# Kernel optimization log

Measured on AMD Instinct MI355X. Metric: run time of the kernel, lower is better.

Reference implementation:

```python
import jax, jax.numpy as jnp
import numpy as np

# ---- config (mirrors DVE_loss.__init__ defaults used here) ----
POW = 0.5
TEMPERATURE = 1.0
SINK_TAU = 0.3      # sink_tau[1]
SINK_ITERS = 30     # sink_iters[1]
LAMBDA_LC = 1.0
SCALE = 20.0        # F.normalize(...) * 20
EPS = 1e-12


def _l2norm(x, axis):
    n = jnp.sqrt(jnp.sum(x * x, axis=axis, keepdims=True))
    return x / jnp.maximum(n, EPS)


def _sinkhorn(log_alpha, tau, n_iters):
    # log-space Sinkhorn normalization (gumbel_sinkhorn with n_samples=1, no noise)
    la = log_alpha / tau
    def body(i, la):
        la = la - jax.nn.logsumexp(la, axis=1, keepdims=True)  # row normalize
        la = la - jax.nn.logsumexp(la, axis=0, keepdims=True)  # col normalize
        return la
    la = jax.lax.fori_loop(0, n_iters, body, la)
    return jnp.exp(la)


def _per_sample(f1, f2, fa, x1):
    # f1, f2, fa: [N, C] (already normalized * 20); x1: [N, 3]
    N = f1.shape[0]
    dt = f1.dtype

    corr_1a = (f1 @ fa.T) / TEMPERATURE                # [N, N]
    smcorr_1a = jax.nn.softmax(corr_1a, axis=1)
    f1_via_fa_t = smcorr_1a @ fa                        # [N, C] (broadcast-weighted sum)
    corr_1a2 = (f1_via_fa_t @ f2.T) / TEMPERATURE       # [N, N]
    smcorr_1a2 = jax.nn.softmax(corr_1a2, axis=1)

    # no-grad sinkhorn target
    sink = jax.lax.stop_gradient(_sinkhorn(corr_1a2, SINK_TAU, SINK_ITERS))

    # pairwise distance matrix (no-grad): ||xi - xj||^pow
    sq = jnp.sum(x1 * x1, axis=-1)                      # [N]
    d2 = jnp.maximum(sq[:, None] + sq[None, :] - 2.0 * (x1 @ x1.T), 0.0)
    dist = jax.lax.stop_gradient(jnp.sqrt(d2) ** POW)   # [N, N]

    smcorr_12 = jax.nn.softmax((f1 @ f2.T) / TEMPERATURE, axis=1)

    L = dist * smcorr_1a2 + dist * smcorr_12
    loss_b = jnp.sum(L) / N

    perm_to_I_b = 3.0 * jnp.sum(jnp.abs(jnp.eye(N, dtype=dt) - sink)) / N
    Lc_b = 3.0 * jnp.sum(jnp.abs(sink - smcorr_1a2)) / N

    # feature_reconstruction(f1, f1) diagnostic (no-grad)
    g = jax.lax.stop_gradient(f1 @ f1.T)                # [N, N]
    smg = jax.nn.softmax(g / TEMPERATURE, axis=1)
    fv = smg @ jax.lax.stop_gradient(f1)                # [N, C] == (f1 @ smcorr.T).T
    corr2 = fv @ jax.lax.stop_gradient(f1).T            # [N, N] (no temperature div)
    sm2 = jax.nn.softmax(corr2, axis=1)
    d_b = -jnp.sum(jnp.diagonal(sm2)) / N

    match_b = jnp.sum(
        (jnp.argmax(smcorr_1a2, axis=1) == jnp.arange(N)).astype(dt))
    return loss_b, Lc_b, perm_to_I_b, d_b, match_b


def setup_inputs() -> dict:
    key = jax.random.key(0)
    k1, k2 = jax.random.split(key)
    feats = jax.random.normal(k1, (16, 2048, 128), dtype=jnp.float32)
    pc0 = jax.random.normal(k2, (8, 2048, 3), dtype=jnp.float32)
    return {"feats": feats, "pc0": pc0, "epoch": 10}


def reference(feats, pc0, epoch):
    x1 = pc0[..., :3]
    feats1 = feats[0::2]                                # [B, N, C]
    feats2 = feats[1::2]
    B = feats1.shape[0]

    f1 = _l2norm(feats1, axis=-1) * SCALE               # normalize per point
    f2 = _l2norm(feats2, axis=-1) * SCALE
    fa = jnp.roll(f1, -1, axis=0)                       # feats1[(b+1) % B]

    loss_b, Lc_b, perm_b, d_b, match_b = jax.vmap(_per_sample)(f1, f2, fa, x1)

    loss = jnp.sum(loss_b)
    Lc = jnp.sum(Lc_b)
    perm_to_I = jnp.sum(perm_b)
    diff_via_recon = jnp.sum(d_b)
    correct_match = jnp.sum(match_b)

    total_loss = loss + LAMBDA_LC * Lc
    return (total_loss / B, loss / B, Lc / B, perm_to_I / B,
            correct_match / B, diff_via_recon / B)
```

## Files before the change

### kernel.cpp

```cpp
#include <hip/hip_runtime.h>
#include <math.h>

constexpr int B_ = 8;
constexpr int N_ = 2048;
constexpr int D_ = 128;
constexpr long long NDl = (long long)N_ * D_;
constexpr long long NNl = (long long)N_ * N_;
constexpr float INV_TAU = 1.0f / 0.3f;
constexpr float SCALE_ = 20.0f;
constexpr float EPS_ = 1e-12f;

typedef __attribute__((ext_vector_type(8))) short short8;
typedef __attribute__((ext_vector_type(4))) float f32x4;
#define MFMA_BF16 __builtin_amdgcn_mfma_f32_16x16x32_bf16

constexpr size_t FL_F  = (size_t)B_ * NDl;
constexpr size_t FL_NN = (size_t)B_ * NNl;
constexpr size_t FL_V  = (size_t)B_ * N_;

constexpr size_t OFF_SQ   = 0;
constexpr size_t OFF_ROWM = OFF_SQ   + FL_V;
constexpr size_t OFF_ROWZ = OFF_ROWM + FL_V;
constexpr size_t OFF_U0   = OFF_ROWZ + FL_V;
constexpr size_t OFF_V0   = OFF_U0   + FL_V;
constexpr size_t OFF_DIAG = OFF_V0   + FL_V;
constexpr size_t OFF_AV   = OFF_DIAG + FL_V;
constexpr size_t OFF_BV   = OFF_AV   + FL_V;
constexpr size_t OFF_ACC  = OFF_BV   + FL_V;
constexpr size_t OFF_PM   = OFF_ACC  + 16;
constexpr size_t OFF_PS   = OFF_PM   + 32 * FL_V;
constexpr size_t OFF_PT   = OFF_PS   + 32 * FL_V;
constexpr size_t OFF_CP   = OFF_PM;
constexpr size_t OFF_PCM  = OFF_PT;
constexpr size_t OFF_PCS  = OFF_PT + 16 * FL_V;
constexpr size_t OFF_C    = OFF_PM + 128 * FL_V;
constexpr size_t OFF_K    = OFF_C  + FL_NN;
constexpr size_t OFF_BF   = OFF_K  + FL_NN / 2;

__device__ inline float bf2f(unsigned int lo16) {
  return __uint_as_float(lo16 << 16);
}
__device__ inline unsigned int f2bf(float x) {
  unsigned int u = __float_as_uint(x);
  u += 0x7fffu + ((u >> 16) & 1u);
  return (u >> 16) & 0xffffu;
}

__device__ inline void gload16(const unsigned short* g, unsigned short* lbase, int lane) {
#if defined(__has_builtin)
#if __has_builtin(__builtin_amdgcn_global_load_lds)
  __builtin_amdgcn_global_load_lds(
      (const __attribute__((address_space(1))) unsigned int*)g,
      (__attribute__((address_space(3))) unsigned int*)lbase, 16, 0, 0);
  return;
#endif
#endif
  *(uint4*)(lbase + lane * 8) = *(const uint4*)g;
}

__global__ __launch_bounds__(64) void k_norm(const float* __restrict__ feats,
                                             unsigned short* __restrict__ f1hi,
                                             unsigned short* __restrict__ f1lo,
                                             unsigned short* __restrict__ f2hi,
                                             unsigned short* __restrict__ f2lo) {
  int r = blockIdx.x, b = blockIdx.y, which = blockIdx.z;
  const float* src = feats + ((size_t)(2 * b + which)) * NDl + (size_t)r * D_;
  int t = threadIdx.x;
  float2 x = *(const float2*)(src + 2 * t);
  float ss = x.x * x.x + x.y * x.y;
#pragma unroll
  for (int off = 32; off; off >>= 1) ss += __shfl_down(ss, off);
  ss = __shfl(ss, 0);
  float s = SCALE_ / fmaxf(sqrtf(ss), EPS_);
  float y0 = x.x * s, y1 = x.y * s;
  unsigned int h0 = f2bf(y0), h1 = f2bf(y1);
  unsigned int l0 = f2bf(y0 - bf2f(h0)), l1 = f2bf(y1 - bf2f(h1));
  size_t o = (size_t)b * NDl + (size_t)r * D_ + 2 * t;
  unsigned short* hb = (which ? f2hi : f1hi);
  unsigned short* lb = (which ? f2lo : f1lo);
  *(unsigned int*)(hb + o) = h0 | (h1 << 16);
  *(unsigned int*)(lb + o) = l0 | (l1 << 16);
}

__global__ __launch_bounds__(256) void k_transpose(const unsigned short* __restrict__ hi,
                                                   const unsigned short* __restrict__ lo,
                                                   unsigned short* __restrict__ thi,
                                                   unsigned short* __restrict__ tlo) {
  __shared__ unsigned short tile[64][66];
  int rt = blockIdx.x, dt = blockIdx.y, z = blockIdx.z;
  int b = z >> 1;
  const unsigned short* s = ((z & 1) ? lo : hi) + (size_t)b * NDl;
  unsigned short* d = ((z & 1) ? tlo : thi) + (size_t)b * NDl;
  int t = threadIdx.x;
  int r = t >> 2, c0 = (t & 3) * 16;
#pragma unroll
  for (int h = 0; h < 2; ++h) {
    uint4 v = *(const uint4*)(s + (size_t)(rt * 64 + r) * D_ + dt * 64 + c0 + h * 8);
    unsigned short* p = &tile[r][c0 + h * 8];
    p[0] = (unsigned short)v.x; p[1] = (unsigned short)(v.x >> 16);
    p[2] = (unsigned short)v.y; p[3] = (unsigned short)(v.y >> 16);
    p[4] = (unsigned short)v.z; p[5] = (unsigned short)(v.z >> 16);
    p[6] = (unsigned short)v.w; p[7] = (unsigned short)(v.w >> 16);
  }
  __syncthreads();
  int dd = t >> 2, r0 = (t & 3) * 16;
#pragma unroll
  for (int h = 0; h < 2; ++h) {
    unsigned int q[4];
#pragma unroll
    for (int e = 0; e < 4; ++e) {
      unsigned short a0 = tile[r0 + h * 8 + 2 * e][dd];
      unsigned short a1 = tile[r0 + h * 8 + 2 * e + 1][dd];
      q[e] = (unsigned int)a0 | ((unsigned int)a1 << 16);
    }
    uint4 v; v.x = q[0]; v.y = q[1]; v.z = q[2]; v.w = q[3];
    *(uint4*)(d + (size_t)(dt * 64 + dd) * N_ + rt * 64 + r0 + h * 8) = v;
  }
}

__global__ __launch_bounds__(256) void k_sq(const float* __restrict__ pc0,
                                            float* __restrict__ sq) {
  int i = blockIdx.x * 256 + threadIdx.x;
  if (i < B_ * N_) {
    float x = pc0[3 * i], y = pc0[3 * i + 1], z = pc0[3 * i + 2];
    sq[i] = x * x + y * y + z * z;
  }
}

template<bool WRITEC, bool TAU, bool SD, bool DIAG>
__global__ __launch_bounds__(256, 2) void k_mm(
    const unsigned short* __restrict__ Ahi_g, const unsigned short* __restrict__ Alo_g,
    const unsigned short* __restrict__ Bhi_g, const unsigned short* __restrict__ Blo_g,
    float* __restrict__ Cb, int roll,
    float* __restrict__ pms, float* __restrict__ pss, float* __restrict__ pts,
    float* __restrict__ diagb,
    const float* __restrict__ pc0, const float* __restrict__ sqv) {
  int bm = blockIdx.x, bn = blockIdx.y, z = blockIdx.z;
  int zb = (z + roll) & 7;
  const unsigned short* A_hi = Ahi_g + (size_t)z * NDl;
  const unsigned short* A_lo = Alo_g + (size_t)z * NDl;
  const unsigned short* B_hi = Bhi_g + (size_t)zb * NDl;
  const unsigned short* B_lo = Blo_g + (size_t)zb * NDl;
  float* C = Cb + (size_t)z * NNl;

  __shared__ __align__(16) unsigned short sAh[128 * 64], sAl[128 * 64];
  __shared__ __align__(16) unsigned short sBh[128 * 64], sBl[128 * 64];
  __shared__ float rpx[128], rpy[128], rpz[128], rps[128];
  __shared__ float cqx[128], cqy[128], cqz[128], cqs[128];

  int t = threadIdx.x;
  int lane = t & 63, w = t >> 6;
  int wm = w >> 1, wn = w & 1;

  if constexpr (SD) {
    const float* xb = pc0 + (size_t)z * N_ * 3;
    const float* sb = sqv + (size_t)z * N_;
    if (t < 128) {
      int r = bm * 128 + t;
      rpx[t] = xb[3 * r]; rpy[t] = xb[3 * r + 1]; rpz[t] = xb[3 * r + 2]; rps[t] = sb[r];
    } else {
      int c = bn * 128 + (t - 128);
      cqx[t - 128] = xb[3 * c]; cqy[t - 128] = xb[3 * c + 1]; cqz[t - 128] = xb[3 * c + 2];
      cqs[t - 128] = sb[c];
    }
  }

  f32x4 acc[4][4] = {};

  for (int kc = 0; kc < D_; kc += 64) {
    if (kc) __syncthreads();
#pragma unroll
    for (int i = 0; i < 4; ++i) {
      int li = i * 256 + t;
      int r = li >> 3;
      int j = li & 7;
      int xoff = (j * 8) ^ ((r & 7) << 3);
      size_t grow_a = (size_t)(bm * 128 + r) * D_ + kc + xoff;
      size_t grow_b = (size_t)(bn * 128 + r) * D_ + kc + xoff;
      int wbase = (i * 256 + (t & 192)) * 8;
      gload16(A_hi + grow_a, &sAh[wbase], lane);
      gload16(A_lo + grow_a, &sAl[wbase], lane);
      gload16(B_hi + grow_b, &sBh[wbase], lane);
      gload16(B_lo + grow_b, &sBl[wbase], lane);
    }
    __syncthreads();

    short8 ah[4][2], al[4][2];
#pragma unroll
    for (int m = 0; m < 4; ++m)
#pragma unroll
      for (int ks = 0; ks < 2; ++ks) {
        int row = wm * 64 + m * 16 + (lane & 15);
        int kb = ks * 64 + ((lane >> 4) * 16);
        int idx = (row * 128 + (kb ^ ((row & 7) << 4))) >> 1;
        ah[m][ks] = *(const short8*)(&sAh[idx]);
        al[m][ks] = *(const short8*)(&sAl[idx]);
      }
#pragma unroll
    for (int n = 0; n < 4; ++n) {
#pragma unroll
      for (int ks = 0; ks < 2; ++ks) {
        int row = wn * 64 + n * 16 + (lane & 15);
        int kb = ks * 64 + ((lane >> 4) * 16);
        int idx = (row * 128 + (kb ^ ((row & 7) << 4))) >> 1;
        short8 bh = *(const short8*)(&sBh[idx]);
        short8 bl = *(const short8*)(&sBl[idx]);
#pragma unroll
        for (int m = 0; m < 4; ++m) {
          acc[m][n] = MFMA_BF16(ah[m][ks], bh, acc[m][n], 0, 0, 0);
          acc[m][n] = MFMA_BF16(ah[m][ks], bl, acc[m][n], 0, 0, 0);
          acc[m][n] = MFMA_BF16(al[m][ks], bh, acc[m][n], 0, 0, 0);
        }
      }
    }
  }

  int lrow = (lane >> 4) * 4;
  int lcol = lane & 15;

  if constexpr (WRITEC) {
#pragma unroll
    for (int m = 0; m < 4; ++m) {
      int gr0 = bm * 128 + wm * 64 + m * 16 + lrow;
#pragma unroll
      for (int n = 0; n < 4; ++n) {
        int gc = bn * 128 + wn * 64 + n * 16 + lcol;
        float* Cp = C + (size_t)gr0 * N_ + gc;
#pragma unroll
        for (int rg = 0; rg < 4; ++rg)
          Cp[(size_t)rg * N_] = acc[m][n][rg];
      }
    }
  }

#pragma unroll
  for (int m = 0; m < 4; ++m) {
#pragma unroll
    for (int rg = 0; rg < 4; ++rg) {
      int rib = wm * 64 + m * 16 + lrow + rg;
      float v0 = acc[m][0][rg], v1 = acc[m][1][rg], v2 = acc[m][2][rg], v3 = acc[m][3][rg];
      float mx = fmaxf(fmaxf(v0, v1), fmaxf(v2, v3));
#pragma unroll
      for (int msk = 1; msk < 16; msk <<= 1) mx = fmaxf(mx, __shfl_xor(mx, msk));
      float e0 = __expf(v0 - mx), e1 = __expf(v1 - mx), e2 = __expf(v2 - mx), e3 = __expf(v3 - mx);
      float s = e0 + e1 + e2 + e3;
      float st = 0.f, sd = 0.f;
      if constexpr (TAU)
        st = __expf((v0 - mx) * INV_TAU) + __expf((v1 - mx) * INV_TAU) +
             __expf((v2 - mx) * INV_TAU) + __expf((v3 - mx) * INV_TAU);
      if constexpr (SD) {
        float xi = rpx[rib], yi = rpy[rib], zi = rpz[rib], si = rps[rib];
#pragma unroll
        for (int n = 0; n < 4; ++n) {
          int ci = wn * 64 + n * 16 + lcol;
          float d2 = fmaxf(si + cqs[ci] - 2.f * (xi * cqx[ci] + yi * cqy[ci] + zi * cqz[ci]), 0.f);
          float en = (n == 0) ? e0 : (n == 1) ? e1 : (n == 2) ? e2 : e3;
          sd += en * sqrtf(sqrtf(d2));
        }
      }
#pragma unroll
      for (int msk = 1; msk < 16; msk <<= 1) {
        s += __shfl_xor(s, msk);
        if constexpr (TAU) st += __shfl_xor(st, msk);
        if constexpr (SD) sd += __shfl_xor(sd, msk);
      }
      if (lcol == 0) {
        size_t idx = ((size_t)(z * 32 + bn * 2 + wn)) * N_ + bm * 128 + rib;
        pms[idx] = mx; pss[idx] = s;
        if constexpr (TAU) pts[idx] = st;
        if constexpr (SD) pts[idx] = sd;
      }
    }
  }

  if constexpr (DIAG) {
    if (bm == bn && wm == wn) {
#pragma unroll
      for (int m = 0; m < 4; ++m)
#pragma unroll
        for (int rg = 0; rg < 4; ++rg) {
          int rr = lrow + rg;
          if (lcol == rr)
            diagb[(size_t)z * N_ + bm * 128 + wm * 64 + m * 16 + rr] = acc[m][m][rg];
        }
    }
  }
}

template<bool WMZ, bool TAU, bool SD, bool DIAG, bool MATCH>
__global__ __launch_bounds__(256) void k_comb(const float* __restrict__ pms,
                                              const float* __restrict__ pss,
                                              const float* __restrict__ pts,
                                              const float* __restrict__ diagb,
                                              float* __restrict__ rowm,
                                              float* __restrict__ rowZ,
                                              float* __restrict__ u0,
                                              float* __restrict__ acc) {
  int b = blockIdx.y;
  int r = blockIdx.x * 256 + threadIdx.x;
  float M = -INFINITY, S = 0.f, ST = 0.f, SDa = 0.f;
#pragma unroll
  for (int p = 0; p < 32; ++p) {
    size_t idx = ((size_t)(b * 32 + p)) * N_ + r;
    float m = pms[idx], s = pss[idx];
    float M2 = fmaxf(M, m);
    float f0 = __expf(M - M2), f1 = __expf(m - M2);
    S = S * f0 + s * f1;
    if constexpr (TAU) ST = ST * __expf((M - M2) * INV_TAU) + pts[idx] * __expf((m - M2) * INV_TAU);
    if constexpr (SD)  SDa = SDa * f0 + pts[idx] * f1;
    M = M2;
  }
  size_t vr = (size_t)b * N_ + r;
  if constexpr (WMZ) { rowm[vr] = M; rowZ[vr] = S; }
  if constexpr (TAU) u0[vr] = M * INV_TAU + __logf(ST);
  float contrib = 0.f; int slot = -1;
  if constexpr (SD)    { contrib = SDa / S; slot = 0; }
  if constexpr (DIAG)  { contrib = __expf(diagb[vr] - M) / S; slot = 3; }
  if constexpr (MATCH) { contrib = (diagb[vr] == M) ? 1.f : 0.f; slot = 4; }
  if (slot >= 0) {
    __shared__ float red[256];
    int t = threadIdx.x;
    red[t] = contrib; __syncthreads();
    for (int off = 128; off; off >>= 1) { if (t < off) red[t] += red[t + off]; __syncthreads(); }
    if (t == 0) atomicAdd(acc + slot, red[0]);
  }
}

__global__ __launch_bounds__(256, 3) void k_smmm(
    const float* __restrict__ Cb, const float* __restrict__ rowm, const float* __restrict__ rowZ,
    const unsigned short* __restrict__ Wthi, const unsigned short* __restrict__ Wtlo,
    unsigned short* __restrict__ Ohi, unsigned short* __restrict__ Olo, int roll) {
  int bm = blockIdx.x, z = blockIdx.y;
  int zb = (z + roll) & 7;
  const float* C = Cb + (size_t)z * NNl + (size_t)(bm * 64) * N_;
  const unsigned short* Wh = Wthi + (size_t)zb * NDl;
  const unsigned short* Wl = Wtlo + (size_t)zb * NDl;

  __shared__ __align__(16) unsigned short sPh[64 * 64], sPl[64 * 64];
  __shared__ __align__(16) unsigned short sWh[128 * 64], sWl[128 * 64];
  __shared__ float s_rm[64], s_rz[64];

  int t = threadIdx.x, lane = t & 63, w = t >> 6;
  if (t < 64) {
    s_rm[t] = rowm[(size_t)z * N_ + bm * 64 + t];
    s_rz[t] = rowZ[(size_t)z * N_ + bm * 64 + t];
  }
  __syncthreads();

  f32x4 acc[8] = {};

  for (int jc = 0; jc < N_; jc += 64) {
    if (jc) __syncthreads();
#pragma unroll
    for (int i = 0; i < 4; ++i) {
      int li = i * 256 + t;
      int r = li >> 4;
      int j4 = (li & 15) * 4;
      float4 c4 = *(const float4*)(C + (size_t)r * N_ + jc + j4);
      float rm = s_rm[r];
      float p0 = __expf(c4.x - rm), p1 = __expf(c4.y - rm);
      float p2 = __expf(c4.z - rm), p3 = __expf(c4.w - rm);
      unsigned int h0 = f2bf(p0), h1 = f2bf(p1), h2 = f2bf(p2), h3 = f2bf(p3);
      unsigned int l0 = f2bf(p0 - bf2f(h0)), l1 = f2bf(p1 - bf2f(h1));
      unsigned int l2 = f2bf(p2 - bf2f(h2)), l3 = f2bf(p3 - bf2f(h3));
      int kb = j4 * 2;
      int sidx = (r * 128 + (kb ^ ((r & 7) << 4))) >> 1;
      uint2 ph; ph.x = h0 | (h1 << 16); ph.y = h2 | (h3 << 16);
      uint2 pl; pl.x = l0 | (l1 << 16); pl.y = l2 | (l3 << 16);
      *(uint2*)(&sPh[sidx]) = ph;
      *(uint2*)(&sPl[sidx]) = pl;
    }
#pragma unroll
    for (int i = 0; i < 4; ++i) {
      int li = i * 256 + t;
      int d = li >> 3;
      int j = li & 7;
      int xoff = (j * 8) ^ ((d & 7) << 3);
      size_t ga = (size_t)d * N_ + jc + xoff;
      int wbase = (i * 256 + (t & 192)) * 8;
      gload16(Wh + ga, &sWh[wbase], lane);
      gload16(Wl + ga, &sWl[wbase], lane);
    }
    __syncthreads();

    short8 ph[2], pl[2];
#pragma unroll
    for (int ks = 0; ks < 2; ++ks) {
      int row = w * 16 + (lane & 15);
      int kb = ks * 64 + ((lane >> 4) * 16);
      int idx = (row * 128 + (kb ^ ((row & 7) << 4))) >> 1;
      ph[ks] = *(const short8*)(&sPh[idx]);
      pl[ks] = *(const short8*)(&sPl[idx]);
    }
#pragma unroll
    for (int n = 0; n < 8; ++n) {
#pragma unroll
      for (int ks = 0; ks < 2; ++ks) {
        int row = n * 16 + (lane & 15);
        int kb = ks * 64 + ((lane >> 4) * 16);
        int idx = (row * 128 + (kb ^ ((row & 7) << 4))) >> 1;
        short8 bh = *(const short8*)(&sWh[idx]);
        short8 bl = *(const short8*)(&sWl[idx]);
        acc[n] = MFMA_BF16(ph[ks], bh, acc[n], 0, 0, 0);
        acc[n] = MFMA_BF16(ph[ks], bl, acc[n], 0, 0, 0);
        acc[n] = MFMA_BF16(pl[ks], bh, acc[n], 0, 0, 0);
      }
    }
  }

  unsigned short* OhB = Ohi + (size_t)z * NDl;
  unsigned short* OlB = Olo + (size_t)z * NDl;
#pragma unroll
  for (int rg = 0; rg < 4; ++rg) {
    int rib = w * 16 + (lane >> 4) * 4 + rg;
    float iZ = 1.f / s_rz[rib];
    size_t ro = (size_t)(bm * 64 + rib) * D_;
#pragma unroll
    for (int n = 0; n < 8; ++n) {
      int d = n * 16 + (lane & 15);
      float vv = acc[n][rg] * iZ;
      unsigned int h = f2bf(vv);
      OhB[ro + d] = (unsigned short)h;
      OlB[ro + d] = (unsigned short)f2bf(vv - bf2f(h));
    }
  }
}

__global__ __launch_bounds__(256) void k_colLSE(const float* __restrict__ Cb,
                                                const float* __restrict__ u0,
                                                float* __restrict__ pcm,
                                                float* __restrict__ pcs) {
  int jb = blockIdx.x, ch = blockIdx.y, b = blockIdx.z;
  int t = threadIdx.x;
  int j4 = (jb * 256 + t) * 4;
  __shared__ float su[128];
  if (t < 128) su[t] = u0[(size_t)b * N_ + ch * 128 + t];
  __syncthreads();
  const float* Cp = Cb + (size_t)b * NNl + (size_t)(ch * 128) * N_ + j4;
  float m0 = -INFINITY, m1 = -INFINITY, m2 = -INFINITY, m3 = -INFINITY;
  float s0 = 0.f, s1 = 0.f, s2 = 0.f, s3 = 0.f;
#pragma unroll 4
  for (int i = 0; i < 128; ++i) {
    float4 c = *(const float4*)(Cp + (size_t)i * N_);
    float ui = su[i];
    float x0 = c.x * INV_TAU - ui, x1 = c.y * INV_TAU - ui;
    float x2 = c.z * INV_TAU - ui, x3 = c.w * INV_TAU - ui;
    float M0 = fmaxf(m0, x0); s0 = s0 * __expf(m0 - M0) + __expf(x0 - M0); m0 = M0;
    float M1 = fmaxf(m1, x1); s1 = s1 * __expf(m1 - M1) + __expf(x1 - M1); m1 = M1;
    float M2 = fmaxf(m2, x2); s2 = s2 * __expf(m2 - M2) + __expf(x2 - M2); m2 = M2;
    float M3 = fmaxf(m3, x3); s3 = s3 * __expf(m3 - M3) + __expf(x3 - M3); m3 = M3;
  }
  size_t o = ((size_t)(b * 16 + ch)) * N_ + j4;
  float4 vm; vm.x = m0; vm.y = m1; vm.z = m2; vm.w = m3;
  float4 vs; vs.x = s0; vs.y = s1; vs.z = s2; vs.w = s3;
  *(float4*)(pcm + o) = vm;
  *(float4*)(pcs + o) = vs;
}

__global__ __launch_bounds__(256) void k_colLSEcomb(const float* __restrict__ pcm,
                                                    const float* __restrict__ pcs,
                                                    float* __restrict__ v0) {
  int b = blockIdx.y; int j = blockIdx.x * 256 + threadIdx.x;
  float m = -INFINITY, s = 0.f;
#pragma unroll
  for (int ch = 0; ch < 16; ++ch) {
    size_t idx = ((size_t)(b * 16 + ch)) * N_ + j;
    float m2 = pcm[idx], s2 = pcs[idx];
    float M = fmaxf(m, m2);
    s = s * __expf(m - M) + s2 * __expf(m2 - M);
    m = M;
  }
  v0[(size_t)b * N_ + j] = m + __logf(s);
}

__global__ __launch_bounds__(256) void k_sink_init(const float* __restrict__ Cb,
                                                   unsigned short* __restrict__ Kp,
                                                   const float* __restrict__ u0,
                                                   const float* __restrict__ v0,
                                                   float* __restrict__ avec,
                                                   float* __restrict__ cp) {
  int stripe = blockIdx.x, b = blockIdx.y;
  int i0 = stripe * 16;
  int t = threadIdx.x;
  int w = t >> 6, l = t & 63;
  __shared__ float a_s[16];
  float bv[4][8];
  const float* vsrc = v0 + (size_t)b * N_;
#pragma unroll
  for (int c = 0; c < 4; ++c) {
    float4 q0 = *(const float4*)(vsrc + c * 512 + l * 8);
    float4 q1 = *(const float4*)(vsrc + c * 512 + l * 8 + 4);
    bv[c][0] = q0.x; bv[c][1] = q0.y; bv[c][2] = q0.z; bv[c][3] = q0.w;
    bv[c][4] = q1.x; bv[c][5] = q1.y; bv[c][6] = q1.z; bv[c][7] = q1.w;
  }
  unsigned short* Kb = Kp + (size_t)b * NNl;
  const float* Cbb = Cb + (size_t)b * NNl;
#pragma unroll
  for (int ii = 0; ii < 4; ++ii) {
    int i = w * 4 + ii;
    int row = i0 + i;
    float r = 0.f;
    float ub = u0[(size_t)b * N_ + row];
    const float* Crow = Cbb + (size_t)row * N_;
    unsigned short* Krow = Kb + (size_t)row * N_;
#pragma unroll
    for (int c = 0; c < 4; ++c) {
      float4 c0 = *(const float4*)(Crow + c * 512 + l * 8);
      float4 c1 = *(const float4*)(Crow + c * 512 + l * 8 + 4);
      float cv[8] = {c0.x, c0.y, c0.z, c0.w, c1.x, c1.y, c1.z, c1.w};
      float kv[8];
#pragma unroll
      for (int e = 0; e < 8; ++e) { kv[e] = __expf(cv[e] * INV_TAU - ub - bv[c][e]); r += kv[e]; }
      uint4 pk;
      pk.x = f2bf(kv[0]) | (f2bf(kv[1]) << 16);
      pk.y = f2bf(kv[2]) | (f2bf(kv[3]) << 16);
      pk.z = f2bf(kv[4]) | (f2bf(kv[5]) << 16);
      pk.w = f2bf(kv[6]) | (f2bf(kv[7]) << 16);
      *(uint4*)(Krow + c * 512 + l * 8) = pk;
    }
#pragma unroll
    for (int off = 1; off < 64; off <<= 1) r += __shfl_xor(r, off);
    if (l == 0) {
      float a = 1.f / r;
      a_s[i] = a;
      avec[(size_t)b * N_ + row] = a;
    }
  }
  __threadfence_block();
  __syncthreads();
  float cpa[8] = {};
  const unsigned short* Kc = Kb + (size_t)i0 * N_ + w * 512 + l * 8;
#pragma unroll 4
  for (int i = 0; i < 16; ++i) {
    uint4 pk = *(const uint4*)(Kc + (size_t)i * N_);
    float ai = a_s[i];
    cpa[0] += bf2f(pk.x & 0xffffu) * ai; cpa[1] += bf2f(pk.x >> 16) * ai;
    cpa[2] += bf2f(pk.y & 0xffffu) * ai; cpa[3] += bf2f(pk.y >> 16) * ai;
    cpa[4] += bf2f(pk.z & 0xffffu) * ai; cpa[5] += bf2f(pk.z >> 16) * ai;
    cpa[6] += bf2f(pk.w & 0xffffu) * ai; cpa[7] += bf2f(pk.w >> 16) * ai;
  }
  size_t o = ((size_t)(b * 128 + stripe)) * N_ + w * 512 + l * 8;
  float4 o0; o0.x = cpa[0]; o0.y = cpa[1]; o0.z = cpa[2]; o0.w = cpa[3];
  float4 o1; o1.x = cpa[4]; o1.y = cpa[5]; o1.z = cpa[6]; o1.w = cpa[7];
  *(float4*)(cp + o) = o0;
  *(float4*)(cp + o + 4) = o1;
}

__global__ __launch_bounds__(256) void k_sink_iterL(const unsigned short* __restrict__ Kp,
                                                    const float* __restrict__ bvec,
                                                    float* __restrict__ avec,
                                                    float* __restrict__ cp) {
  int stripe = blockIdx.x, b = blockIdx.y;
  int i0 = stripe * 16;
  int t = threadIdx.x;
  int w = t >> 6, l = t & 63;
  __shared__ __align__(16) unsigned short sK[16 * 2048];
  __shared__ float a_s[16];
  const unsigned short* Kb = Kp + (size_t)b * NNl + (size_t)i0 * N_;
#pragma unroll
  for (int i = 0; i < 16; ++i) {
    int li = i * 256 + t;
    int row = li >> 8;
    int j = li & 255;
    int wbase = (i * 256 + (t & 192)) * 8;
    gload16(Kb + (size_t)row * N_ + j * 8, &sK[wbase], l);
  }
  float bv[4][8];
  const float* vsrc = bvec + (size_t)b * N_;
#pragma unroll
  for (int c = 0; c < 4; ++c) {
    float4 q0 = *(const float4*)(vsrc + c * 512 + l * 8);
    float4 q1 = *(const float4*)(vsrc + c * 512 + l * 8 + 4);
    bv[c][0] = q0.x; bv[c][1] = q0.y; bv[c][2] = q0.z; bv[c][3] = q0.w;
    bv[c][4] = q1.x; bv[c][5] = q1.y; bv[c][6] = q1.z; bv[c][7] = q1.w;
  }
  __syncthreads();
#pragma unroll
  for (int ii = 0; ii < 4; ++ii) {
    int i = w * 4 + ii;
    float r = 0.f;
#pragma unroll
    for (int c = 0; c < 4; ++c) {
      uint4 pk = *(const uint4*)(&sK[i * 2048 + c * 512 + l * 8]);
      r += bf2f(pk.x & 0xffffu) * bv[c][0] + bf2f(pk.x >> 16) * bv[c][1]
         + bf2f(pk.y & 0xffffu) * bv[c][2] + bf2f(pk.y >> 16) * bv[c][3]
         + bf2f(pk.z & 0xffffu) * bv[c][4] + bf2f(pk.z >> 16) * bv[c][5]
         + bf2f(pk.w & 0xffffu) * bv[c][6] + bf2f(pk.w >> 16) * bv[c][7];
    }
#pragma unroll
    for (int off = 1; off < 64; off <<= 1) r += __shfl_xor(r, off);
    if (l == 0) {
      float a = 1.f / r;
      a_s[i] = a;
      avec[(size_t)b * N_ + i0 + i] = a;
    }
  }
  __syncthreads();
  float cpa[8] = {};
#pragma unroll 4
  for (int i = 0; i < 16; ++i) {
    uint4 pk = *(const uint4*)(&sK[i * 2048 + w * 512 + l * 8]);
    float ai = a_s[i];
    cpa[0] += bf2f(pk.x & 0xffffu) * ai; cpa[1] += bf2f(pk.x >> 16) * ai;
    cpa[2] += bf2f(pk.y & 0xffffu) * ai; cpa[3] += bf2f(pk.y >> 16) * ai;
    cpa[4] += bf2f(pk.z & 0xffffu) * ai; cpa[5] += bf2f(pk.z >> 16) * ai;
    cpa[6] += bf2f(pk.w & 0xffffu) * ai; cpa[7] += bf2f(pk.w >> 16) * ai;
  }
  size_t o = ((size_t)(b * 128 + stripe)) * N_ + w * 512 + l * 8;
  float4 o0; o0.x = cpa[0]; o0.y = cpa[1]; o0.z = cpa[2]; o0.w = cpa[3];
  float4 o1; o1.x = cpa[4]; o1.y = cpa[5]; o1.z = cpa[6]; o1.w = cpa[7];
  *(float4*)(cp + o) = o0;
  *(float4*)(cp + o + 4) = o1;
}

__global__ __launch_bounds__(256) void k_bcomb(const float* __restrict__ cp,
                                               float* __restrict__ bvec) {
  int b = blockIdx.y; int j = blockIdx.x * 256 + threadIdx.x;
  float s0 = 0.f, s1 = 0.f, s2 = 0.f, s3 = 0.f;
#pragma unroll 8
  for (int st = 0; st < 128; st += 4) {
    s0 += cp[((size_t)(b * 128 + st + 0)) * N_ + j];
    s1 += cp[((size_t)(b * 128 + st + 1)) * N_ + j];
    s2 += cp[((size_t)(b * 128 + st + 2)) * N_ + j];
    s3 += cp[((size_t)(b * 128 + st + 3)) * N_ + j];
  }
  bvec[(size_t)b * N_ + j] = 1.f / ((s0 + s1) + (s2 + s3));
}

__global__ __launch_bounds__(256) void k_felem(const float* __restrict__ Cb,
                                               const unsigned short* __restrict__ Kp,
                                               const float* __restrict__ rowm,
                                               const float* __restrict__ rowZ,
                                               const float* __restrict__ avec,
                                               const float* __restrict__ bvec,
                                               const float* __restrict__ pc0,
                                               const float* __restrict__ sqv,
                                               float* __restrict__ acc) {
  int rb = blockIdx.x, b = blockIdx.y;
  int i0 = rb * 16;
  int t = threadIdx.x;
  const float* xb = pc0 + (size_t)b * N_ * 3;
  const float* sqb = sqv + (size_t)b * N_;
  float xj[2][4], yj[2][4], zj[2][4], sj[2][4], bj[2][4];
#pragma unroll
  for (int kk = 0; kk < 2; ++kk) {
    int j4 = t * 4 + kk * 1024;
    float4 p0 = *(const float4*)(xb + 3 * j4);
    float4 p1 = *(const float4*)(xb + 3 * j4 + 4);
    float4 p2 = *(const float4*)(xb + 3 * j4 + 8);
    xj[kk][0] = p0.x; yj[kk][0] = p0.y; zj[kk][0] = p0.z;
    xj[kk][1] = p0.w; yj[kk][1] = p1.x; zj[kk][1] = p1.y;
    xj[kk][2] = p1.z; yj[kk][2] = p1.w; zj[kk][2] = p2.x;
    xj[kk][3] = p2.y; yj[kk][3] = p2.z; zj[kk][3] = p2.w;
    float4 s4 = *(const float4*)(sqb + j4);
    sj[kk][0] = s4.x; sj[kk][1] = s4.y; sj[kk][2] = s4.z; sj[kk][3] = s4.w;
    float4 b4 = *(const float4*)(bvec + (size_t)b * N_ + j4);
    bj[kk][0] = b4.x; bj[kk][1] = b4.y; bj[kk][2] = b4.z; bj[kk][3] = b4.w;
  }
  float aL = 0.f, aLc = 0.f, aP = 0.f;
  for (int ii = 0; ii < 16; ++ii) {
    int i = i0 + ii;
    float xi = xb[3 * i], yi = xb[3 * i + 1], zi = xb[3 * i + 2];
    float sqi = sqb[i];
    float mi = rowm[(size_t)b * N_ + i];
    float iZ = 1.f / rowZ[(size_t)b * N_ + i];
    float ai = avec[(size_t)b * N_ + i];
    const float* Crow = Cb + (size_t)b * NNl + (size_t)i * N_;
    const unsigned short* Krow = Kp + (size_t)b * NNl + (size_t)i * N_;
#pragma unroll
    for (int kk = 0; kk < 2; ++kk) {
      int j4 = t * 4 + kk * 1024;
      float4 c4 = *(const float4*)(Crow + j4);
      uint2 k2 = *(const uint2*)(Krow + j4);
      float kf[4] = { bf2f(k2.x & 0xffffu), bf2f(k2.x >> 16),
                      bf2f(k2.y & 0xffffu), bf2f(k2.y >> 16) };
      float cf[4] = { c4.x, c4.y, c4.z, c4.w };
#pragma unroll
      for (int e = 0; e < 4; ++e) {
        int j = j4 + e;
        float sm = __expf(cf[e] - mi) * iZ;
        float sink = kf[e] * ai * bj[kk][e];
        float d2 = fmaxf(sqi + sj[kk][e] - 2.f * (xi * xj[kk][e] + yi * yj[kk][e] + zi * zj[kk][e]), 0.f);
        aL += sqrtf(sqrtf(d2)) * sm;
        aLc += fabsf(sink - sm);
        aP += fabsf(((i == j) ? 1.f : 0.f) - sink);
      }
    }
  }
  __shared__ float red[256];
  red[t] = aL; __syncthreads();
  for (int off = 128; off; off >>= 1) { if (t < off) red[t] += red[t + off]; __syncthreads(); }
  if (t == 0) atomicAdd(acc + 0, red[0]);
  __syncthreads();
  red[t] = aLc; __syncthreads();
  for (int off = 128; off; off >>= 1) { if (t < off) red[t] += red[t + off]; __syncthreads(); }
  if (t == 0) atomicAdd(acc + 1, red[0]);
  __syncthreads();
  red[t] = aP; __syncthreads();
  for (int off = 128; off; off >>= 1) { if (t < off) red[t] += red[t + off]; __syncthreads(); }
  if (t == 0) atomicAdd(acc + 2, red[0]);
}

__global__ void k_finalize(const float* __restrict__ acc, float* __restrict__ out) {
  float invN = 1.0f / (float)N_;
  float L  = acc[0] * invN;
  float Lc = 3.f * acc[1] * invN;
  float P  = 3.f * acc[2] * invN;
  float Dg = -acc[3] * invN;
  float M  = acc[4];
  float invB = 1.0f / (float)B_;
  out[0] = (L + Lc) * invB;
  out[1] = L * invB;
  out[2] = Lc * invB;
  out[3] = P * invB;
  out[4] = M * invB;
  out[5] = Dg * invB;
}

extern "C" void kernel_launch(void* const* d_in, const int* in_sizes, int n_in,
                              void* d_out, int out_size, void* d_ws, size_t ws_size,
                              hipStream_t stream) {
  const float* feats = (const float*)d_in[0];
  const float* pc0 = (const float*)d_in[1];
  float* out = (float*)d_out;
  float* ws = (float*)d_ws;

  float* sqv   = ws + OFF_SQ;
  float* rowm  = ws + OFF_ROWM;
  float* rowZ  = ws + OFF_ROWZ;
  float* u0    = ws + OFF_U0;
  float* v0    = ws + OFF_V0;
  float* diagb = ws + OFF_DIAG;
  float* avec  = ws + OFF_AV;
  float* bvec  = ws + OFF_BV;
  float* acc   = ws + OFF_ACC;
  float* pms   = ws + OFF_PM;
  float* pss   = ws + OFF_PS;
  float* pts   = ws + OFF_PT;
  float* pcm   = ws + OFF_PCM;
  float* pcs   = ws + OFF_PCS;
  float* cp    = ws + OFF_CP;
  float* C     = ws + OFF_C;
  unsigned short* Kp = (unsigned short*)(ws + OFF_K);
  unsigned short* bfb = (unsigned short*)(ws + OFF_BF);
  unsigned short* f1hi   = bfb + 0 * FL_F;
  unsigned short* f1lo   = bfb + 1 * FL_F;
  unsigned short* f2hi   = bfb + 2 * FL_F;
  unsigned short* f2lo   = bfb + 3 * FL_F;
  unsigned short* f1t_hi = bfb + 4 * FL_F;
  unsigned short* f1t_lo = bfb + 5 * FL_F;
  unsigned short* fvahi  = bfb + 6 * FL_F;
  unsigned short* fvalo  = bfb + 7 * FL_F;

  hipMemsetAsync(acc, 0, 16 * sizeof(float), stream);

  k_norm<<<dim3(N_, B_, 2), 64, 0, stream>>>(feats, f1hi, f1lo, f2hi, f2lo);
  k_transpose<<<dim3(32, 2, 16), 256, 0, stream>>>(f1hi, f1lo, f1t_hi, f1t_lo);
  k_sq<<<(B_ * N_) / 256, 256, 0, stream>>>(pc0, sqv);

  dim3 mmGrid(N_ / 128, N_ / 128, B_);
  dim3 cbGrid(N_ / 256, B_);
  dim3 smGrid(N_ / 64, B_);

  k_mm<true, false, false, false><<<mmGrid, 256, 0, stream>>>(f1hi, f1lo, f1hi, f1lo, C, 0, pms, pss, pts, diagb, pc0, sqv);
  k_comb<true, false, false, false, false><<<cbGrid, 256, 0, stream>>>(pms, pss, pts, diagb, rowm, rowZ, u0, acc);
  k_smmm<<<smGrid, 256, 0, stream>>>(C, rowm, rowZ, f1t_hi, f1t_lo, fvahi, fvalo, 0);
  k_mm<false, false, false, true><<<mmGrid, 256, 0, stream>>>(fvahi, fvalo, f1hi, f1lo, C, 0, pms, pss, pts, diagb, pc0, sqv);
  k_comb<false, false, false, true, false><<<cbGrid, 256, 0, stream>>>(pms, pss, pts, diagb, rowm, rowZ, u0, acc);

  k_mm<false, false, true, false><<<mmGrid, 256, 0, stream>>>(f1hi, f1lo, f2hi, f2lo, C, 0, pms, pss, pts, diagb, pc0, sqv);
  k_comb<false, false, true, false, false><<<cbGrid, 256, 0, stream>>>(pms, pss, pts, diagb, rowm, rowZ, u0, acc);

  k_mm<true, false, false, false><<<mmGrid, 256, 0, stream>>>(f1hi, f1lo, f1hi, f1lo, C, 1, pms, pss, pts, diagb, pc0, sqv);
  k_comb<true, false, false, false, false><<<cbGrid, 256, 0, stream>>>(pms, pss, pts, diagb, rowm, rowZ, u0, acc);
  k_smmm<<<smGrid, 256, 0, stream>>>(C, rowm, rowZ, f1t_hi, f1t_lo, fvahi, fvalo, 1);

  k_mm<true, true, false, true><<<mmGrid, 256, 0, stream>>>(fvahi, fvalo, f2hi, f2lo, C, 0, pms, pss, pts, diagb, pc0, sqv);
  k_comb<true, true, false, false, true><<<cbGrid, 256, 0, stream>>>(pms, pss, pts, diagb, rowm, rowZ, u0, acc);

  k_colLSE<<<dim3(2, 16, B_), 256, 0, stream>>>(C, u0, pcm, pcs);
  k_colLSEcomb<<<cbGrid, 256, 0, stream>>>(pcm, pcs, v0);
  k_sink_init<<<dim3(128, B_), 256, 0, stream>>>(C, Kp, u0, v0, avec, cp);
  k_bcomb<<<cbGrid, 256, 0, stream>>>(cp, bvec);
  for (int it = 0; it < 28; ++it) {
    k_sink_iterL<<<dim3(128, B_), 256, 0, stream>>>(Kp, bvec, avec, cp);
    k_bcomb<<<cbGrid, 256, 0, stream>>>(cp, bvec);
  }

  k_felem<<<dim3(N_ / 16, B_), 256, 0, stream>>>(C, Kp, rowm, rowZ, avec, bvec, pc0, sqv, acc);

  k_finalize<<<1, 1, 0, stream>>>(acc, out);
}
```

Before: 1.460 ms.

## Replace per-iteration Sinkhorn kernel launches with persistent kernel using grid barriers

Swaps 28 pairs of Sinkhorn iteration and column-combine launches for one persistent kernel of 256 blocks of 1024 threads. Each block owns a 64-row stripe of one batch's K matrix, processes it in four 16-row chunks, and uses a global atomic barrier to hand off the column-sum combine step. This removes launch overhead and partial-sum traffic across 56 launches. In exchange it relies on all 256 blocks being co-resident for the spin barrier, and it still reloads K from global memory on every iteration.

```diff
diff --git a/kernel.cpp b/kernel.cpp
--- a/kernel.cpp
+++ b/kernel.cpp
@@ -56,6 +56,24 @@
 #endif
 #endif
   *(uint4*)(lbase + lane * 8) = *(const uint4*)g;
+}
+
+__device__ inline void gbar(int* cnt, int* gen, int nblocks, int target) {
+  __syncthreads();
+  if (threadIdx.x == 0) {
+    __threadfence();
+    int t = __hip_atomic_fetch_add(cnt, 1, __ATOMIC_ACQ_REL, __HIP_MEMORY_SCOPE_AGENT);
+    if (t == nblocks - 1) {
+      __hip_atomic_store(cnt, 0, __ATOMIC_RELAXED, __HIP_MEMORY_SCOPE_AGENT);
+      __hip_atomic_fetch_add(gen, 1, __ATOMIC_ACQ_REL, __HIP_MEMORY_SCOPE_AGENT);
+    } else {
+      while (__hip_atomic_load(gen, __ATOMIC_ACQUIRE, __HIP_MEMORY_SCOPE_AGENT) < target) {
+        __builtin_amdgcn_s_sleep(2);
+      }
+    }
+    __threadfence();
+  }
+  __syncthreads();
 }
 
 __global__ __launch_bounds__(64) void k_norm(const float* __restrict__ feats,
@@ -546,73 +564,6 @@
   *(float4*)(cp + o + 4) = o1;
 }
 
-__global__ __launch_bounds__(256) void k_sink_iterL(const unsigned short* __restrict__ Kp,
-                                                    const float* __restrict__ bvec,
-                                                    float* __restrict__ avec,
-                                                    float* __restrict__ cp) {
-  int stripe = blockIdx.x, b = blockIdx.y;
-  int i0 = stripe * 16;
-  int t = threadIdx.x;
-  int w = t >> 6, l = t & 63;
-  __shared__ __align__(16) unsigned short sK[16 * 2048];
-  __shared__ float a_s[16];
-  const unsigned short* Kb = Kp + (size_t)b * NNl + (size_t)i0 * N_;
-#pragma unroll
-  for (int i = 0; i < 16; ++i) {
-    int li = i * 256 + t;
-    int row = li >> 8;
-    int j = li & 255;
-    int wbase = (i * 256 + (t & 192)) * 8;
-    gload16(Kb + (size_t)row * N_ + j * 8, &sK[wbase], l);
-  }
-  float bv[4][8];
-  const float* vsrc = bvec + (size_t)b * N_;
-#pragma unroll
-  for (int c = 0; c < 4; ++c) {
-    float4 q0 = *(const float4*)(vsrc + c * 512 + l * 8);
-    float4 q1 = *(const float4*)(vsrc + c * 512 + l * 8 + 4);
-    bv[c][0] = q0.x; bv[c][1] = q0.y; bv[c][2] = q0.z; bv[c][3] = q0.w;
-    bv[c][4] = q1.x; bv[c][5] = q1.y; bv[c][6] = q1.z; bv[c][7] = q1.w;
-  }
-  __syncthreads();
-#pragma unroll
-  for (int ii = 0; ii < 4; ++ii) {
-    int i = w * 4 + ii;
-    float r = 0.f;
-#pragma unroll
-    for (int c = 0; c < 4; ++c) {
-      uint4 pk = *(const uint4*)(&sK[i * 2048 + c * 512 + l * 8]);
-      r += bf2f(pk.x & 0xffffu) * bv[c][0] + bf2f(pk.x >> 16) * bv[c][1]
-         + bf2f(pk.y & 0xffffu) * bv[c][2] + bf2f(pk.y >> 16) * bv[c][3]
-         + bf2f(pk.z & 0xffffu) * bv[c][4] + bf2f(pk.z >> 16) * bv[c][5]
-         + bf2f(pk.w & 0xffffu) * bv[c][6] + bf2f(pk.w >> 16) * bv[c][7];
-    }
-#pragma unroll
-    for (int off = 1; off < 64; off <<= 1) r += __shfl_xor(r, off);
-    if (l == 0) {
-      float a = 1.f / r;
-      a_s[i] = a;
-      avec[(size_t)b * N_ + i0 + i] = a;
-    }
-  }
-  __syncthreads();
-  float cpa[8] = {};
-#pragma unroll 4
-  for (int i = 0; i < 16; ++i) {
-    uint4 pk = *(const uint4*)(&sK[i * 2048 + w * 512 + l * 8]);
-    float ai = a_s[i];
-    cpa[0] += bf2f(pk.x & 0xffffu) * ai; cpa[1] += bf2f(pk.x >> 16) * ai;
-    cpa[2] += bf2f(pk.y & 0xffffu) * ai; cpa[3] += bf2f(pk.y >> 16) * ai;
-    cpa[4] += bf2f(pk.z & 0xffffu) * ai; cpa[5] += bf2f(pk.z >> 16) * ai;
-    cpa[6] += bf2f(pk.w & 0xffffu) * ai; cpa[7] += bf2f(pk.w >> 16) * ai;
-  }
-  size_t o = ((size_t)(b * 128 + stripe)) * N_ + w * 512 + l * 8;
-  float4 o0; o0.x = cpa[0]; o0.y = cpa[1]; o0.z = cpa[2]; o0.w = cpa[3];
-  float4 o1; o1.x = cpa[4]; o1.y = cpa[5]; o1.z = cpa[6]; o1.w = cpa[7];
-  *(float4*)(cp + o) = o0;
-  *(float4*)(cp + o + 4) = o1;
-}
-
 __global__ __launch_bounds__(256) void k_bcomb(const float* __restrict__ cp,
                                                float* __restrict__ bvec) {
   int b = blockIdx.y; int j = blockIdx.x * 256 + threadIdx.x;
@@ -625,6 +576,82 @@
     s3 += cp[((size_t)(b * 128 + st + 3)) * N_ + j];
   }
   bvec[(size_t)b * N_ + j] = 1.f / ((s0 + s1) + (s2 + s3));
+}
+
+__global__ __launch_bounds__(1024, 1) void k_sink_pers(
+    const unsigned short* __restrict__ Kp,
+    float* __restrict__ bvec,
+    float* __restrict__ avec,
+    float* __restrict__ cp, int iters,
+    int* bar_cnt, int* bar_gen) {
+  int blk = blockIdx.x;
+  int b = blk >> 5, rc = blk & 31;
+  int t = threadIdx.x;
+  int w = t >> 6, l = t & 63;
+  __shared__ __align__(16) unsigned short sK[16 * 2048];
+  __shared__ float a_s[16];
+  const unsigned short* Kb = Kp + (size_t)b * NNl + (size_t)(rc * 64) * N_;
+  int barnum = 0;
+
+  for (int it = 0; it < iters; ++it) {
+    float bv[4][8];
+    const float* vsrc = bvec + (size_t)b * N_;
+#pragma unroll
+    for (int c = 0; c < 4; ++c) {
+      float4 q0 = *(const float4*)(vsrc + c * 512 + l * 8);
+      float4 q1 = *(const float4*)(vsrc + c * 512 + l * 8 + 4);
+      bv[c][0] = q0.x; bv[c][1] = q0.y; bv[c][2] = q0.z; bv[c][3] = q0.w;
+      bv[c][4] = q1.x; bv[c][5] = q1.y; bv[c][6] = q1.z; bv[c][7] = q1.w;
+    }
+    float cpa0 = 0.f, cpa1 = 0.f;
+    for (int ch = 0; ch < 4; ++ch) {
+      __syncthreads();
+#pragma unroll
+      for (int i = 0; i < 4; ++i) {
+        int li = i * 1024 + t;
+        int wbase = (li & ~63) * 8;
+        gload16(Kb + (size_t)(ch * 16) * N_ + (size_t)li * 8, &sK[wbase], l);
+      }
+      __syncthreads();
+      float r = 0.f;
+#pragma unroll
+      for (int c = 0; c < 4; ++c) {
+        uint4 pk = *(const uint4*)(&sK[w * 2048 + c * 512 + l * 8]);
+        r += bf2f(pk.x & 0xffffu) * bv[c][0] + bf2f(pk.x >> 16) * bv[c][1]
+           + bf2f(pk.y & 0xffffu) * bv[c][2] + bf2f(pk.y >> 16) * bv[c][3]
+           + bf2f(pk.z & 0xffffu) * bv[c][4] + bf2f(pk.z >> 16) * bv[c][5]
+           + bf2f(pk.w & 0xffffu) * bv[c][6] + bf2f(pk.w >> 16) * bv[c][7];
+      }
+#pragma unroll
+      for (int off = 1; off < 64; off <<= 1) r += __shfl_xor(r, off);
+      if (l == 0) {
+        float a = 1.f / r;
+        a_s[w] = a;
+        avec[(size_t)b * N_ + rc * 64 + ch * 16 + w] = a;
+      }
+      __syncthreads();
+#pragma unroll
+      for (int i = 0; i < 16; ++i) {
+        unsigned int u = *(const unsigned int*)(&sK[i * 2048 + 2 * t]);
+        float ai = a_s[i];
+        cpa0 += bf2f(u & 0xffffu) * ai;
+        cpa1 += bf2f(u >> 16) * ai;
+      }
+    }
+    float2 o2; o2.x = cpa0; o2.y = cpa1;
+    *(float2*)(cp + ((size_t)(b * 32 + rc)) * N_ + 2 * t) = o2;
+    gbar(bar_cnt, bar_gen, 256, ++barnum);
+    if (t < 64) {
+      int b2 = blk >> 5;
+      int j = (blk & 31) * 64 + t;
+      float s = 0.f;
+#pragma unroll
+      for (int st = 0; st < 32; ++st)
+        s += cp[((size_t)(b2 * 32 + st)) * N_ + j];
+      bvec[(size_t)b2 * N_ + j] = 1.f / s;
+    }
+    gbar(bar_cnt, bar_gen, 256, ++barnum);
+  }
 }
 
 __global__ __launch_bounds__(256) void k_felem(const float* __restrict__ Cb,
@@ -751,6 +778,8 @@
   unsigned short* f1t_lo = bfb + 5 * FL_F;
   unsigned short* fvahi  = bfb + 6 * FL_F;
   unsigned short* fvalo  = bfb + 7 * FL_F;
+  int* bar_cnt = (int*)(acc + 8);
+  int* bar_gen = (int*)(acc + 9);
 
   hipMemsetAsync(acc, 0, 16 * sizeof(float), stream);
 
@@ -782,10 +811,7 @@
   k_colLSEcomb<<<cbGrid, 256, 0, stream>>>(pcm, pcs, v0);
   k_sink_init<<<dim3(128, B_), 256, 0, stream>>>(C, Kp, u0, v0, avec, cp);
   k_bcomb<<<cbGrid, 256, 0, stream>>>(cp, bvec);
-  for (int it = 0; it < 28; ++it) {
-    k_sink_iterL<<<dim3(128, B_), 256, 0, stream>>>(Kp, bvec, avec, cp);
-    k_bcomb<<<cbGrid, 256, 0, stream>>>(cp, bvec);
-  }
+  k_sink_pers<<<dim3(256), dim3(1024), 0, stream>>>(Kp, bvec, avec, cp, 28, bar_cnt, bar_gen);
 
   k_felem<<<dim3(N_ / 16, B_), 256, 0, stream>>>(C, Kp, rowm, rowZ, avec, bvec, pc0, sqv, acc);
 
```

Measured after the change: 3.219 ms. 2.2x slower.
